# Performance work log

Measured on AMD Instinct MI355X. Metric: run time of the kernel, lower is better.

The kernel has to match this reference:

```python
import jax, jax.numpy as jnp
import numpy as np
import math

NSEG = 4
SAMPLE_RATE = 16  # curve samples per bezier segment
SHARPNESS = 150.0


def _control_radians():
    n = NSEG
    theta = math.pi * 2 / (4 * n) + math.atan(math.tan(2 * math.pi / (4 * n)) / 3)
    r = []
    for i in range(n):
        r += [2 * math.pi / n * i, 2 * math.pi / n * i + theta, 2 * math.pi / n * (i + 1) - theta]
    return jnp.asarray(np.asarray(r, dtype=np.float32).reshape(n, 3))


def sdf_extruded_bezier(quaternion, translation, points, control_polygon, bez_weights, height):
    # quaternion [B,K,4], translation [B,K,3], points [B,M,3],
    # control_polygon [B,K,nseg,3,2], bez_weights [B,K,nseg,2], height [B,K]
    B, K, _ = quaternion.shape
    p = points[:, :, None, :] - translation[:, None, :, :]            # [B,M,K,3]
    q = quaternion[:, None, :, :]
    qn = q / jnp.sqrt(jnp.sum(q * q, -1, keepdims=True) + 1e-8)
    w, qv = qn[..., :1], -qn[..., 1:]                                  # conjugate -> world->local
    t2 = 2.0 * jnp.cross(qv, p)
    pl = p + w * t2 + jnp.cross(qv, t2)                                # local coords [B,M,K,3]
    p2d, pz = pl[..., :2], pl[..., 2]
    # rational cubic bezier per segment: P0,P1,P2 from this segment, P3 = next segment's P0
    P0 = control_polygon[:, :, :, 0, :]
    P1 = control_polygon[:, :, :, 1, :]
    P2 = control_polygon[:, :, :, 2, :]
    P3 = jnp.roll(P0, -1, axis=2)
    ts = jnp.linspace(0.0, 1.0, SAMPLE_RATE, endpoint=False)           # [S]
    b0 = (1 - ts) ** 3
    b1 = 3 * (1 - ts) ** 2 * ts
    b2 = 3 * (1 - ts) * ts ** 2
    b3 = ts ** 3
    w1 = bez_weights[..., 0:1]                                          # [B,K,nseg,1]
    w2 = bez_weights[..., 1:2]
    den = b0 + w1 * b1 + w2 * b2 + b3                                   # [B,K,nseg,S]
    num = (P0[..., None, :] * b0[:, None]
           + P1[..., None, :] * (w1[..., None] * b1[:, None])
           + P2[..., None, :] * (w2[..., None] * b2[:, None])
           + P3[..., None, :] * b3[:, None])                            # [B,K,nseg,S,2]
    curve = (num / den[..., None]).reshape(B, K, NSEG * SAMPLE_RATE, 2)
    rel = curve[:, None] - p2d[..., None, :]                            # [B,M,K,S*nseg,2]
    d2 = jnp.sum(rel * rel, -1)
    dmin = jnp.sqrt(jnp.min(d2, -1) + 1e-12)                            # unsigned 2D distance
    nxt = jnp.roll(rel, -1, axis=-2)
    cross = rel[..., 0] * nxt[..., 1] - rel[..., 1] * nxt[..., 0]
    dot = jnp.sum(rel * nxt, -1)
    winding = jnp.sum(jnp.arctan2(cross, dot), -1) / (2 * math.pi)
    sdf2d = jnp.where(jnp.abs(winding) > 0.5, -dmin, dmin)
    dz = jnp.abs(pz) - jnp.abs(height)[:, None, :]
    sdf = (jnp.minimum(jnp.maximum(sdf2d, dz), 0.0)
           + jnp.sqrt(jnp.maximum(sdf2d, 0.0) ** 2 + jnp.maximum(dz, 0.0) ** 2 + 1e-12))
    return sdf, dmin


def setup_inputs() -> dict:
    key = jax.random.key(0)
    k1, k2, k3, k4 = jax.random.split(key, 4)
    B, M, K, C = 4, 2048, 64, 64
    P = 4 + 3 + 1 + NSEG * 3 + NSEG * 2  # 28
    return {
        "sample_point_coordinates": jax.random.uniform(k1, (B, M, 3), jnp.float32, -1.0, 1.0),
        "primitive_parameters": 0.3 * jax.random.normal(k2, (B, P, K), jnp.float32),
        "intersection_layer_weights": jax.random.uniform(k3, (B, K, C), jnp.float32),
        "union_layer_weights": jax.random.uniform(k4, (B, C), jnp.float32),
        "is_training": 1,
    }


def reference(sample_point_coordinates, primitive_parameters, intersection_layer_weights, union_layer_weights, is_training):
    pp = jnp.swapaxes(primitive_parameters, 1, 2)                       # [B,K,P]
    B, K, _ = pp.shape
    quaternion = pp[..., :4]
    translation = pp[..., 4:7]
    height = pp[..., 7]
    radius = jnp.abs(pp[..., 8:8 + NSEG * 3]).reshape(B, K, NSEG, 3)
    rad = _control_radians()[None, None]                                # [1,1,nseg,3]
    control_polygon = jnp.stack([jnp.cos(rad) * radius, jnp.sin(rad) * radius], -1)
    bez_weights = jnp.abs(pp[..., 8 + NSEG * 3:]).reshape(B, K, NSEG, 2)
    primitive_sdf, support_distances = sdf_extruded_bezier(
        quaternion, translation, sample_point_coordinates, control_polygon, bez_weights, height)
    primitive_occ = jax.nn.sigmoid(-primitive_sdf * SHARPNESS)          # [B,M,K]
    # occupancy_pre_intersection = w*occ + (1-w)*1 = 1 - w*(1-occ), fused
    w_int = intersection_layer_weights[:, None]                         # [B,1,K,C]
    pre_i = 1.0 - w_int * (1.0 - primitive_occ[..., None])              # [B,M,K,C]
    if is_training:
        sw = jax.lax.stop_gradient(jax.nn.softmax(pre_i * -40.0, axis=-2))
        inter = jnp.sum(sw * pre_i, -2)                                 # soft-min -> [B,M,C]
    else:
        inter = jnp.min(pre_i, -2)
    pre_u = union_layer_weights[:, None, :] * inter
    if is_training:
        sw2 = jax.lax.stop_gradient(jax.nn.softmax(pre_u * 40.0, axis=-1))
        occupancies = jnp.sum(sw2 * pre_u, -1)                          # soft-max -> [B,M]
    else:
        occupancies = jnp.max(pre_u, -1)
    return occupancies, primitive_sdf, inter, support_distances
```

## Files before the change

### kernel.cpp

```cpp
#include <hip/hip_runtime.h>
#include <math.h>


#define NB 4
#define NM 2048
#define NK 64
#define NC 64
#define NS 64
#define PPB 4

#define OCC_OFF   0
#define SDF_OFF   8192
#define INTER_OFF 532480
#define SUP_OFF   1056768

#define CT 0.86285621096f
#define ST 0.50544946275f

#define L2E_40  57.70780163555852f
#define L2E_150 216.40425613334447f

__global__ __launch_bounds__(256) void extrude_net_kernel(
    const float* __restrict__ pts,
    const float* __restrict__ pp,
    const float* __restrict__ Wint,
    const float* __restrict__ Uw,
    float* __restrict__ out)
{
    __shared__ float2 s_curve[NS][NK];
    __shared__ float  s_om[PPB][NK];

    const int tid  = threadIdx.x;
    const int lane = tid & 63;
    const int wv   = tid >> 6;
    const int gpt  = blockIdx.x * PPB + wv;
    const int b    = gpt >> 11;
    const float* __restrict__ ppb = pp + b * (28 * NK);

    {
        const int k    = lane;
        const int seg  = wv;
        const int nseg = (seg + 1) & 3;
        const float r0 = fabsf(ppb[(8 + seg * 3 + 0) * NK + k]);
        const float r1 = fabsf(ppb[(8 + seg * 3 + 1) * NK + k]);
        const float r2 = fabsf(ppb[(8 + seg * 3 + 2) * NK + k]);
        const float rn = fabsf(ppb[(8 + nseg * 3 + 0) * NK + k]);
        const float w1 = fabsf(ppb[(20 + seg * 2 + 0) * NK + k]);
        const float w2 = fabsf(ppb[(20 + seg * 2 + 1) * NK + k]);

        const float c0x[4] = { 1.f, 0.f, -1.f,  0.f };
        const float c0y[4] = { 0.f, 1.f,  0.f, -1.f };
        const float c1x[4] = {  CT, -ST, -CT,  ST };
        const float c1y[4] = {  ST,  CT, -ST, -CT };
        const float c2x[4] = {  ST, -CT, -ST,  CT };
        const float c2y[4] = {  CT,  ST, -CT, -ST };

        const float P0x = c0x[seg] * r0,  P0y = c0y[seg] * r0;
        const float P1x = c1x[seg] * r1,  P1y = c1y[seg] * r1;
        const float P2x = c2x[seg] * r2,  P2y = c2y[seg] * r2;
        const float P3x = c0x[nseg] * rn, P3y = c0y[nseg] * rn;

        #pragma unroll
        for (int j = 0; j < 16; ++j) {
            const float t  = (float)j * 0.0625f;
            const float u  = 1.f - t;
            const float b0 = u * u * u;
            const float b1 = 3.f * u * u * t;
            const float b2 = 3.f * u * t * t;
            const float b3 = t * t * t;
            const float wb1 = w1 * b1, wb2 = w2 * b2;
            const float inv = __builtin_amdgcn_rcpf(b0 + wb1 + wb2 + b3);
            const int s = seg * 16 + j;
            s_curve[s][k] = make_float2(
                (P0x * b0 + P1x * wb1 + P2x * wb2 + P3x * b3) * inv,
                (P0y * b0 + P1y * wb1 + P2y * wb2 + P3y * b3) * inv);
        }
    }
    __syncthreads();

    const float ptx = pts[gpt * 3 + 0];
    const float pty = pts[gpt * 3 + 1];
    const float ptz = pts[gpt * 3 + 2];
    {
        const int k = lane;
        const float q0 = ppb[0 * NK + k], q1 = ppb[1 * NK + k];
        const float q2 = ppb[2 * NK + k], q3 = ppb[3 * NK + k];
        const float trx = ppb[4 * NK + k], try_ = ppb[5 * NK + k], trz = ppb[6 * NK + k];
        const float h   = ppb[7 * NK + k];

        const float px = ptx - trx, py = pty - try_, pz = ptz - trz;
        const float inv = 1.f / sqrtf(q0 * q0 + q1 * q1 + q2 * q2 + q3 * q3 + 1e-8f);
        const float w  = q0 * inv;
        const float vx = -q1 * inv, vy = -q2 * inv, vz = -q3 * inv;
        const float t2x = 2.f * (vy * pz - vz * py);
        const float t2y = 2.f * (vz * px - vx * pz);
        const float t2z = 2.f * (vx * py - vy * px);
        const float plx = px + w * t2x + (vy * t2z - vz * t2y);
        const float ply = py + w * t2y + (vz * t2x - vx * t2z);
        const float plz = pz + w * t2z + (vx * t2y - vy * t2x);

        float2 c0 = s_curve[0][k];
        float rx = c0.x - plx;
        float ry = c0.y - ply;
        int   wn    = 0;
        float d2min = 3.4e38f;
        #pragma unroll 8
        for (int s = 0; s < NS; ++s) {
            const int sn = (s + 1) & 63;
            const float2 cn = s_curve[sn][k];
            const float nx = cn.x - plx;
            const float ny = cn.y - ply;
            const float cr = rx * ny - ry * nx;
            wn += (ry <= 0.f && ny >  0.f && cr > 0.f) ? 1 : 0;
            wn -= (ry >  0.f && ny <= 0.f && cr < 0.f) ? 1 : 0;
            d2min = fminf(d2min, rx * rx + ry * ry);
            rx = nx; ry = ny;
        }
        const float dmin  = sqrtf(d2min + 1e-12f);
        const float sdf2d = (wn != 0) ? -dmin : dmin;
        const float dz    = fabsf(plz) - fabsf(h);
        const float mx    = fmaxf(sdf2d, dz);
        const float e1    = fmaxf(sdf2d, 0.f);
        const float e2    = fmaxf(dz, 0.f);
        const float sdf   = fminf(mx, 0.f) + sqrtf(e1 * e1 + e2 * e2 + 1e-12f);

        out[SDF_OFF + gpt * NK + k] = sdf;
        out[SUP_OFF + gpt * NK + k] = dmin;
        s_om[wv][k] = 1.f / (1.f + exp2f(-sdf * L2E_150));
    }
    __syncthreads();

    {
        const int c = lane;
        const float* __restrict__ Wb = Wint + b * (NK * NC);
        float srun = 0.f, trun = 0.f;
        #pragma unroll 8
        for (int kk = 0; kk < NK; ++kk) {
            const float om  = s_om[wv][kk];
            const float pre = fmaf(-Wb[kk * NC + c], om, 1.f);
            const float e   = exp2f(pre * -L2E_40);
            srun += e;
            trun = fmaf(e, pre, trun);
        }
        const float inter = trun / srun;
        out[INTER_OFF + gpt * NC + c] = inter;

        const float pu = Uw[b * NC + c] * inter;
        float umax = pu;
        #pragma unroll
        for (int off = 32; off > 0; off >>= 1)
            umax = fmaxf(umax, __shfl_xor(umax, off, 64));
        const float e = exp2f((pu - umax) * L2E_40);
        float s1 = e, s2 = e * pu;
        #pragma unroll
        for (int off = 32; off > 0; off >>= 1) {
            s1 += __shfl_xor(s1, off, 64);
            s2 += __shfl_xor(s2, off, 64);
        }
        if (lane == 0) out[OCC_OFF + gpt] = s2 / s1;
    }
}

extern "C" void kernel_launch(void* const* d_in, const int* in_sizes, int n_in,
                              void* d_out, int out_size, void* d_ws, size_t ws_size,
                              hipStream_t stream) {
    const float* pts  = (const float*)d_in[0];
    const float* pp   = (const float*)d_in[1];
    const float* Wint = (const float*)d_in[2];
    const float* Uw   = (const float*)d_in[3];
    float* out = (float*)d_out;

    const int n_points = NB * NM;
    const int grid     = n_points / PPB;
    extrude_net_kernel<<<grid, 256, 0, stream>>>(pts, pp, Wint, Uw, out);
}
```

Baseline: 91.45 us.

## Precompute bezier curve table in a separate kernel and double points per block

```diff
diff --git a/kernel.cpp b/kernel.cpp
--- a/kernel.cpp
+++ b/kernel.cpp
@@ -7,7 +7,7 @@
 #define NK 64
 #define NC 64
 #define NS 64
-#define PPB 4
+#define PPB 8
 
 #define OCC_OFF   0
 #define SDF_OFF   8192
@@ -20,15 +20,63 @@
 #define L2E_40  57.70780163555852f
 #define L2E_150 216.40425613334447f
 
-__global__ __launch_bounds__(256) void extrude_net_kernel(
+__global__ __launch_bounds__(256) void curve_table_kernel(
+    const float* __restrict__ pp,
+    float2* __restrict__ wcurve)
+{
+    const int b    = blockIdx.x;
+    const int lane = threadIdx.x & 63;
+    const int seg  = threadIdx.x >> 6;
+    const int nseg = (seg + 1) & 3;
+    const float* __restrict__ ppb = pp + b * (28 * NK);
+    const int k = lane;
+
+    const float r0 = fabsf(ppb[(8 + seg * 3 + 0) * NK + k]);
+    const float r1 = fabsf(ppb[(8 + seg * 3 + 1) * NK + k]);
+    const float r2 = fabsf(ppb[(8 + seg * 3 + 2) * NK + k]);
+    const float rn = fabsf(ppb[(8 + nseg * 3 + 0) * NK + k]);
+    const float w1 = fabsf(ppb[(20 + seg * 2 + 0) * NK + k]);
+    const float w2 = fabsf(ppb[(20 + seg * 2 + 1) * NK + k]);
+
+    const float c0x[4] = { 1.f, 0.f, -1.f,  0.f };
+    const float c0y[4] = { 0.f, 1.f,  0.f, -1.f };
+    const float c1x[4] = {  CT, -ST, -CT,  ST };
+    const float c1y[4] = {  ST,  CT, -ST, -CT };
+    const float c2x[4] = {  ST, -CT, -ST,  CT };
+    const float c2y[4] = {  CT,  ST, -CT, -ST };
+
+    const float P0x = c0x[seg] * r0,  P0y = c0y[seg] * r0;
+    const float P1x = c1x[seg] * r1,  P1y = c1y[seg] * r1;
+    const float P2x = c2x[seg] * r2,  P2y = c2y[seg] * r2;
+    const float P3x = c0x[nseg] * rn, P3y = c0y[nseg] * rn;
+
+    #pragma unroll
+    for (int j = 0; j < 16; ++j) {
+        const float t  = (float)j * 0.0625f;
+        const float u  = 1.f - t;
+        const float b0 = u * u * u;
+        const float b1 = 3.f * u * u * t;
+        const float b2 = 3.f * u * t * t;
+        const float b3 = t * t * t;
+        const float wb1 = w1 * b1, wb2 = w2 * b2;
+        const float inv = __builtin_amdgcn_rcpf(b0 + wb1 + wb2 + b3);
+        const int s = seg * 16 + j;
+        wcurve[(b * NS + s) * NK + k] = make_float2(
+            (P0x * b0 + P1x * wb1 + P2x * wb2 + P3x * b3) * inv,
+            (P0y * b0 + P1y * wb1 + P2y * wb2 + P3y * b3) * inv);
+    }
+}
+
+__global__ __launch_bounds__(512, 8) void extrude_net_kernel(
     const float* __restrict__ pts,
     const float* __restrict__ pp,
     const float* __restrict__ Wint,
     const float* __restrict__ Uw,
+    const float2* __restrict__ wcurve,
     float* __restrict__ out)
 {
-    __shared__ float2 s_curve[NS][NK];
-    __shared__ float  s_om[PPB][NK];
+    __shared__ __align__(16) float2 s_curve[NS][NK];
+    __shared__ float s_om[PPB][NK];
 
     const int tid  = threadIdx.x;
     const int lane = tid & 63;
@@ -38,43 +86,11 @@
     const float* __restrict__ ppb = pp + b * (28 * NK);
 
     {
-        const int k    = lane;
-        const int seg  = wv;
-        const int nseg = (seg + 1) & 3;
-        const float r0 = fabsf(ppb[(8 + seg * 3 + 0) * NK + k]);
-        const float r1 = fabsf(ppb[(8 + seg * 3 + 1) * NK + k]);
-        const float r2 = fabsf(ppb[(8 + seg * 3 + 2) * NK + k]);
-        const float rn = fabsf(ppb[(8 + nseg * 3 + 0) * NK + k]);
-        const float w1 = fabsf(ppb[(20 + seg * 2 + 0) * NK + k]);
-        const float w2 = fabsf(ppb[(20 + seg * 2 + 1) * NK + k]);
-
-        const float c0x[4] = { 1.f, 0.f, -1.f,  0.f };
-        const float c0y[4] = { 0.f, 1.f,  0.f, -1.f };
-        const float c1x[4] = {  CT, -ST, -CT,  ST };
-        const float c1y[4] = {  ST,  CT, -ST, -CT };
-        const float c2x[4] = {  ST, -CT, -ST,  CT };
-        const float c2y[4] = {  CT,  ST, -CT, -ST };
-
-        const float P0x = c0x[seg] * r0,  P0y = c0y[seg] * r0;
-        const float P1x = c1x[seg] * r1,  P1y = c1y[seg] * r1;
-        const float P2x = c2x[seg] * r2,  P2y = c2y[seg] * r2;
-        const float P3x = c0x[nseg] * rn, P3y = c0y[nseg] * rn;
-
+        const float4* __restrict__ src = (const float4*)wcurve + b * (NS * NK / 2);
+        float4* dst = (float4*)&s_curve[0][0];
         #pragma unroll
-        for (int j = 0; j < 16; ++j) {
-            const float t  = (float)j * 0.0625f;
-            const float u  = 1.f - t;
-            const float b0 = u * u * u;
-            const float b1 = 3.f * u * u * t;
-            const float b2 = 3.f * u * t * t;
-            const float b3 = t * t * t;
-            const float wb1 = w1 * b1, wb2 = w2 * b2;
-            const float inv = __builtin_amdgcn_rcpf(b0 + wb1 + wb2 + b3);
-            const int s = seg * 16 + j;
-            s_curve[s][k] = make_float2(
-                (P0x * b0 + P1x * wb1 + P2x * wb2 + P3x * b3) * inv,
-                (P0y * b0 + P1y * wb1 + P2y * wb2 + P3y * b3) * inv);
-        }
+        for (int i = 0; i < 4; ++i)
+            dst[i * 512 + tid] = src[i * 512 + tid];
     }
     __syncthreads();
 
@@ -89,7 +105,7 @@
         const float h   = ppb[7 * NK + k];
 
         const float px = ptx - trx, py = pty - try_, pz = ptz - trz;
-        const float inv = 1.f / sqrtf(q0 * q0 + q1 * q1 + q2 * q2 + q3 * q3 + 1e-8f);
+        const float inv = __builtin_amdgcn_rsqf(q0 * q0 + q1 * q1 + q2 * q2 + q3 * q3 + 1e-8f);
         const float w  = q0 * inv;
         const float vx = -q1 * inv, vy = -q2 * inv, vz = -q3 * inv;
         const float t2x = 2.f * (vy * pz - vz * py);
@@ -99,24 +115,37 @@
         const float ply = py + w * t2y + (vz * t2x - vx * t2z);
         const float plz = pz + w * t2z + (vx * t2y - vy * t2x);
 
-        float2 c0 = s_curve[0][k];
-        float rx = c0.x - plx;
-        float ry = c0.y - ply;
-        int   wn    = 0;
-        float d2min = 3.4e38f;
-        #pragma unroll 8
-        for (int s = 0; s < NS; ++s) {
-            const int sn = (s + 1) & 63;
-            const float2 cn = s_curve[sn][k];
+        const float2* __restrict__ col = &s_curve[0][k];
+
+        const float2 cfirst = col[0];
+        float rx = cfirst.x - plx;
+        float ry = cfirst.y - ply;
+        const float r0x = rx, r0y = ry;
+        bool  aflag = ry > 0.f;
+        const bool flag0 = aflag;
+        int   up = 0, dn = 0;
+        float d2a = rx * rx + ry * ry;
+        float d2b = 3.4e38f;
+        #pragma unroll 9
+        for (int s = 1; s < NS; ++s) {
+            const float2 cn = col[s * NK];
             const float nx = cn.x - plx;
             const float ny = cn.y - ply;
             const float cr = rx * ny - ry * nx;
-            wn += (ry <= 0.f && ny >  0.f && cr > 0.f) ? 1 : 0;
-            wn -= (ry >  0.f && ny <= 0.f && cr < 0.f) ? 1 : 0;
-            d2min = fminf(d2min, rx * rx + ry * ry);
-            rx = nx; ry = ny;
-        }
-        const float dmin  = sqrtf(d2min + 1e-12f);
+            const bool  bflag = ny > 0.f;
+            up += (!aflag && bflag && cr > 0.f) ? 1 : 0;
+            dn += (aflag && !bflag && cr < 0.f) ? 1 : 0;
+            const float d2 = nx * nx + ny * ny;
+            if (s & 1) d2b = fminf(d2b, d2); else d2a = fminf(d2a, d2);
+            aflag = bflag; rx = nx; ry = ny;
+        }
+        {
+            const float cr = rx * r0y - ry * r0x;
+            up += (!aflag && flag0 && cr > 0.f) ? 1 : 0;
+            dn += (aflag && !flag0 && cr < 0.f) ? 1 : 0;
+        }
+        const int   wn    = up - dn;
+        const float dmin  = sqrtf(fminf(d2a, d2b) + 1e-12f);
         const float sdf2d = (wn != 0) ? -dmin : dmin;
         const float dz    = fabsf(plz) - fabsf(h);
         const float mx    = fmaxf(sdf2d, dz);
@@ -126,23 +155,24 @@
 
         out[SDF_OFF + gpt * NK + k] = sdf;
         out[SUP_OFF + gpt * NK + k] = dmin;
-        s_om[wv][k] = 1.f / (1.f + exp2f(-sdf * L2E_150));
+        s_om[wv][k] = __builtin_amdgcn_rcpf(1.f + exp2f(-sdf * L2E_150));
     }
     __syncthreads();
 
     {
         const int c = lane;
-        const float* __restrict__ Wb = Wint + b * (NK * NC);
+        const float* __restrict__ Wb  = Wint + b * (NK * NC);
+        const float* __restrict__ omw = s_om[wv];
         float srun = 0.f, trun = 0.f;
         #pragma unroll 8
         for (int kk = 0; kk < NK; ++kk) {
-            const float om  = s_om[wv][kk];
+            const float om  = omw[kk];
             const float pre = fmaf(-Wb[kk * NC + c], om, 1.f);
             const float e   = exp2f(pre * -L2E_40);
             srun += e;
             trun = fmaf(e, pre, trun);
         }
-        const float inter = trun / srun;
+        const float inter = trun * __builtin_amdgcn_rcpf(srun);
         out[INTER_OFF + gpt * NC + c] = inter;
 
         const float pu = Uw[b * NC + c] * inter;
@@ -157,7 +187,7 @@
             s1 += __shfl_xor(s1, off, 64);
             s2 += __shfl_xor(s2, off, 64);
         }
-        if (lane == 0) out[OCC_OFF + gpt] = s2 / s1;
+        if (lane == 0) out[OCC_OFF + gpt] = s2 * __builtin_amdgcn_rcpf(s1);
     }
 }
 
@@ -168,9 +198,10 @@
     const float* pp   = (const float*)d_in[1];
     const float* Wint = (const float*)d_in[2];
     const float* Uw   = (const float*)d_in[3];
-    float* out = (float*)d_out;
-
-    const int n_points = NB * NM;
-    const int grid     = n_points / PPB;
-    extrude_net_kernel<<<grid, 256, 0, stream>>>(pts, pp, Wint, Uw, out);
+    float*  out    = (float*)d_out;
+    float2* wcurve = (float2*)d_ws;
+
+    curve_table_kernel<<<NB, 256, 0, stream>>>(pp, wcurve);
+    const int grid = (NB * NM) / PPB;
+    extrude_net_kernel<<<grid, 512, 0, stream>>>(pts, pp, Wint, Uw, wcurve, out);
 }
```

New measurement: 93.00 us. Within noise of the previous version (+1.7%).
